# Optimization experiments

Measured on AMD Instinct MI355X. Metric: run time of the kernel, lower is better.

Reference implementation:

```python
import jax, jax.numpy as jnp
import numpy as np

HIDDEN = 1024
HEADS = 16
HEAD_DIM = HIDDEN // HEADS
LN_EPS = 1e-5


def setup_inputs() -> dict:
    key = jax.random.key(0)
    ks = jax.random.split(key, 8)
    B, S = 4, 2048
    s = 1.0 / np.sqrt(HIDDEN)
    return {
        "x": jax.random.normal(ks[0], (B, S, HIDDEN), dtype=jnp.float32),
        "Wq": jax.random.normal(ks[1], (HIDDEN, HIDDEN), dtype=jnp.float32) * s,
        "bq": jax.random.normal(ks[2], (HIDDEN,), dtype=jnp.float32) * 0.01,
        "Wk": jax.random.normal(ks[3], (HIDDEN, HIDDEN), dtype=jnp.float32) * s,
        "bk": jax.random.normal(ks[4], (HIDDEN,), dtype=jnp.float32) * 0.01,
        "Wv": jax.random.normal(ks[5], (HIDDEN, HIDDEN), dtype=jnp.float32) * s,
        "bv": jax.random.normal(ks[6], (HIDDEN,), dtype=jnp.float32) * 0.01,
        "gamma": jnp.ones((HIDDEN,), dtype=jnp.float32),
        "beta": jnp.zeros((HIDDEN,), dtype=jnp.float32),
    }


def reference(x, Wq, bq, Wk, bk, Wv, bv, gamma, beta):
    B, S, H = x.shape
    # LayerNorm
    mu = jnp.mean(x, axis=-1, keepdims=True)
    var = jnp.mean(jnp.square(x - mu), axis=-1, keepdims=True)
    xn = (x - mu) / jnp.sqrt(var + LN_EPS) * gamma + beta
    # QKV projections -> [B, heads, S, head_dim]
    def split_heads(t):
        return t.reshape(B, S, HEADS, HEAD_DIM).transpose(0, 2, 1, 3)
    q = split_heads(xn @ Wq + bq)
    k = split_heads(xn @ Wk + bk)
    v = split_heads(xn @ Wv + bv)
    scores = jnp.einsum("bhqd,bhkd->bhqk", q, k) / np.sqrt(HEAD_DIM)
    probs = jax.nn.softmax(scores, axis=-1)
    attended = jnp.einsum("bhqk,bhkd->bhqd", probs, v)
    attended = attended.transpose(0, 2, 1, 3).reshape(B, S, H)
    # residual (dropout = 0.0 / eval mode is identity)
    return xn + attended
```

## Files before the change

kernel.cpp:

```cpp
#include <hip/hip_runtime.h>
#include <hip/hip_bf16.h>

#define HIDDEN 1024
#define HEADS 16
#define HEAD_DIM 64
#define SEQ 2048
#define BATCH 4

typedef __attribute__((ext_vector_type(8))) short bf16x8;
typedef __attribute__((ext_vector_type(4))) float f32x4;
typedef __attribute__((ext_vector_type(16))) float f32x16;
typedef __attribute__((ext_vector_type(4))) short short4v;

static __device__ __forceinline__ unsigned short f2bf(float f) {
  union { float f; unsigned u; } u;
  u.f = f;
  unsigned r = u.u + 0x7fffu + ((u.u >> 16) & 1u);
  return (unsigned short)(r >> 16);
}

static __device__ __forceinline__ unsigned packtr(float lo, float hi) {
  union { float f; unsigned u; } a, b;
  a.f = lo; b.f = hi;
#if __has_builtin(__builtin_amdgcn_perm)
  return __builtin_amdgcn_perm(b.u, a.u, 0x07060302u);
#else
  return (b.u & 0xFFFF0000u) | (a.u >> 16);
#endif
}

static __device__ __forceinline__ bf16x8 frag4(unsigned u0, unsigned u1,
                                               unsigned u2, unsigned u3) {
  union { unsigned u[4]; bf16x8 v; } t;
  t.u[0] = u0; t.u[1] = u1; t.u[2] = u2; t.u[3] = u3;
  return t.v;
}

static __device__ __forceinline__ float fexp2(float x) {
#if __has_builtin(__builtin_amdgcn_exp2f)
  return __builtin_amdgcn_exp2f(x);
#else
  return exp2f(x);
#endif
}

typedef const __attribute__((address_space(1))) unsigned int* gp1_t;
typedef __attribute__((address_space(3))) unsigned int* lp3_t;
static __device__ __forceinline__ void gload_lds16(const void* g, void* l) {
  __builtin_amdgcn_global_load_lds((gp1_t)g, (lp3_t)l, 16, 0, 0);
}

__global__ __launch_bounds__(256) void wtrans_kernel(
    const float* __restrict__ Wq, const float* __restrict__ Wk,
    const float* __restrict__ Wv, unsigned short* __restrict__ Wt) {
  __shared__ float tile[64][65];
  int z = blockIdx.z;
  const float* W = (z == 0) ? Wq : (z == 1) ? Wk : Wv;
  int k0 = blockIdx.x * 64, n0 = blockIdx.y * 64;
  int tid = threadIdx.x;
  int tr = tid >> 4;
  int tc = tid & 15;
#pragma unroll
  for (int p = 0; p < 4; ++p) {
    int kk = p * 16 + tr;
    float4 v = *(const float4*)(W + (size_t)(k0 + kk) * HIDDEN + n0 + tc * 4);
    tile[kk][tc * 4 + 0] = v.x; tile[kk][tc * 4 + 1] = v.y;
    tile[kk][tc * 4 + 2] = v.z; tile[kk][tc * 4 + 3] = v.w;
  }
  __syncthreads();
  unsigned short* op = Wt + (size_t)z * HIDDEN * HIDDEN;
#pragma unroll
  for (int p = 0; p < 4; ++p) {
    int nn = p * 16 + tr;
    short4v o;
    o.x = (short)f2bf(tile[tc * 4 + 0][nn]);
    o.y = (short)f2bf(tile[tc * 4 + 1][nn]);
    o.z = (short)f2bf(tile[tc * 4 + 2][nn]);
    o.w = (short)f2bf(tile[tc * 4 + 3][nn]);
    *(short4v*)(op + (size_t)(n0 + nn) * HIDDEN + k0 + tc * 4) = o;
  }
}

__global__ __launch_bounds__(256) void ln_kernel(
    const float* __restrict__ x, const float* __restrict__ gamma,
    const float* __restrict__ beta, float* __restrict__ out,
    unsigned short* __restrict__ xnb) {
  int row = blockIdx.x;
  int tid = threadIdx.x;
  const float4* xr = (const float4*)(x + (size_t)row * HIDDEN);
  float4 v = xr[tid];
  float s = v.x + v.y + v.z + v.w;
  float sq = v.x * v.x + v.y * v.y + v.z * v.z + v.w * v.w;
#pragma unroll
  for (int off = 32; off >= 1; off >>= 1) {
    s += __shfl_xor(s, off);
    sq += __shfl_xor(sq, off);
  }
  __shared__ float red[8];
  int wave = tid >> 6, lane = tid & 63;
  if (lane == 0) { red[wave] = s; red[4 + wave] = sq; }
  __syncthreads();
  s = red[0] + red[1] + red[2] + red[3];
  sq = red[4] + red[5] + red[6] + red[7];
  float mu = s * (1.0f / HIDDEN);
  float var = sq * (1.0f / HIDDEN) - mu * mu;
  float rstd = rsqrtf(var + 1e-5f);
  float4 g = ((const float4*)gamma)[tid];
  float4 bt = ((const float4*)beta)[tid];
  float4 o;
  o.x = (v.x - mu) * rstd * g.x + bt.x;
  o.y = (v.y - mu) * rstd * g.y + bt.y;
  o.z = (v.z - mu) * rstd * g.z + bt.z;
  o.w = (v.w - mu) * rstd * g.w + bt.w;
  ((float4*)(out + (size_t)row * HIDDEN))[tid] = o;
  short4v p;
  p.x = (short)f2bf(o.x); p.y = (short)f2bf(o.y);
  p.z = (short)f2bf(o.z); p.w = (short)f2bf(o.w);
  *((short4v*)(xnb + (size_t)row * HIDDEN) + tid) = p;
}

__global__ __launch_bounds__(256) void qkv_gemm(
    const unsigned short* __restrict__ xnb, const unsigned short* __restrict__ Wt,
    const float* __restrict__ bq, const float* __restrict__ bk,
    const float* __restrict__ bv, unsigned short* __restrict__ qO,
    unsigned short* __restrict__ kO, unsigned short* __restrict__ vtO) {
  __shared__ unsigned short As[2][128 * 64];
  __shared__ unsigned short Bs[2][128 * 64];
  int z = blockIdx.z;
  int m0 = blockIdx.x * 128;
  int n0 = blockIdx.y * 128;
  int tid = threadIdx.x;
  int wave = tid >> 6, lane = tid & 63;
  int lr = lane & 15, g = lane >> 4;
  int wm = wave >> 1, wn = wave & 1;
  const unsigned short* Ab = xnb + (size_t)m0 * HIDDEN;
  const unsigned short* Bb = Wt + (size_t)z * HIDDEN * HIDDEN + (size_t)n0 * HIDDEN;
  int srow = wave * 8 + (lane >> 3);
  int scol = ((lane & 7) ^ (lane >> 3)) << 3;
  f32x4 acc[4][4];
#pragma unroll
  for (int i = 0; i < 4; ++i)
#pragma unroll
    for (int j = 0; j < 4; ++j) acc[i][j] = (f32x4){0.f, 0.f, 0.f, 0.f};

#pragma unroll
  for (int i = 0; i < 4; ++i) {
    int row = i * 32 + srow;
    gload_lds16(Ab + (size_t)row * HIDDEN + scol, &As[0][(i * 32 + wave * 8) * 64]);
    gload_lds16(Bb + (size_t)row * HIDDEN + scol, &Bs[0][(i * 32 + wave * 8) * 64]);
  }
  __syncthreads();

#pragma unroll 1
  for (int t = 0; t < 16; ++t) {
    int cur = t & 1;
    if (t < 15) {
      int k1 = (t + 1) * 64;
#pragma unroll
      for (int i = 0; i < 4; ++i) {
        int row = i * 32 + srow;
        gload_lds16(Ab + (size_t)row * HIDDEN + k1 + scol, &As[cur ^ 1][(i * 32 + wave * 8) * 64]);
        gload_lds16(Bb + (size_t)row * HIDDEN + k1 + scol, &Bs[cur ^ 1][(i * 32 + wave * 8) * 64]);
      }
    }
    bf16x8 aF[4][2], bF[4][2];
#pragma unroll
    for (int mb = 0; mb < 4; ++mb) {
      int row = wm * 64 + mb * 16 + lr;
#pragma unroll
      for (int ks = 0; ks < 2; ++ks)
        aF[mb][ks] = *(const bf16x8*)&As[cur][row * 64 + (((ks * 4 + g) ^ (row & 7)) << 3)];
    }
#pragma unroll
    for (int nb = 0; nb < 4; ++nb) {
      int row = wn * 64 + nb * 16 + lr;
#pragma unroll
      for (int ks = 0; ks < 2; ++ks)
        bF[nb][ks] = *(const bf16x8*)&Bs[cur][row * 64 + (((ks * 4 + g) ^ (row & 7)) << 3)];
    }
#pragma unroll
    for (int ks = 0; ks < 2; ++ks)
#pragma unroll
      for (int mb = 0; mb < 4; ++mb)
#pragma unroll
        for (int nb = 0; nb < 4; ++nb)
          acc[mb][nb] = __builtin_amdgcn_mfma_f32_16x16x32_bf16(aF[mb][ks], bF[nb][ks], acc[mb][nb], 0, 0, 0);
    __syncthreads();
  }
  const float* bias = (z == 0) ? bq : (z == 1) ? bk : bv;
  if (z == 2) {
#pragma unroll
    for (int nb = 0; nb < 4; ++nb) {
      int n = n0 + wn * 64 + nb * 16 + lr;
      float bsv = bias[n];
      int h = n >> 6, d = n & 63;
#pragma unroll
      for (int mb = 0; mb < 4; ++mb) {
        int m = m0 + wm * 64 + mb * 16 + g * 4;
        int bb = m >> 11, sIdx = m & 2047;
        short4v pk;
        pk.x = (short)f2bf(acc[mb][nb][0] + bsv);
        pk.y = (short)f2bf(acc[mb][nb][1] + bsv);
        pk.z = (short)f2bf(acc[mb][nb][2] + bsv);
        pk.w = (short)f2bf(acc[mb][nb][3] + bsv);
        *(short4v*)(vtO + (size_t)((bb * HEADS + h) * HEAD_DIM + d) * SEQ + sIdx) = pk;
      }
    }
  } else {
    unsigned short* outp = (z == 0) ? qO : kO;
    float scale = (z == 0) ? 0.18033688011112042f : 1.0f;
#pragma unroll
    for (int nb = 0; nb < 4; ++nb) {
      int n = n0 + wn * 64 + nb * 16 + lr;
      float bsv = bias[n];
      int h = n >> 6, d = n & 63;
#pragma unroll
      for (int mb = 0; mb < 4; ++mb) {
#pragma unroll
        for (int r = 0; r < 4; ++r) {
          int m = m0 + wm * 64 + mb * 16 + g * 4 + r;
          int bb = m >> 11, sIdx = m & 2047;
          unsigned short bits = f2bf((acc[mb][nb][r] + bsv) * scale);
          outp[(size_t)((bb * HEADS + h) * SEQ + sIdx) * HEAD_DIM + d] = bits;
        }
      }
    }
  }
}

static __device__ __forceinline__ void attn_subtile(
    const unsigned short* __restrict__ Kb, const unsigned short* __restrict__ Vb,
    const int (&koff)[4], const bf16x8 (&qF)[4],
    const f32x16& ZERO, f32x16& o0, f32x16& o1, float& lsum) {
  f32x16 sc0, sc1;
  __builtin_amdgcn_s_setprio(1);
  {
    bf16x8 k0 = *(const bf16x8*)&Kb[koff[0]];
    bf16x8 k1 = *(const bf16x8*)&Kb[koff[0] + 256];
    sc0 = __builtin_amdgcn_mfma_f32_32x32x16_bf16(k0, qF[0], ZERO, 0, 0, 0);
    sc1 = __builtin_amdgcn_mfma_f32_32x32x16_bf16(k1, qF[0], ZERO, 0, 0, 0);
  }
#pragma unroll
  for (int s = 1; s < 4; ++s) {
    bf16x8 k0 = *(const bf16x8*)&Kb[koff[s]];
    bf16x8 k1 = *(const bf16x8*)&Kb[koff[s] + 256];
    sc0 = __builtin_amdgcn_mfma_f32_32x32x16_bf16(k0, qF[s], sc0, 0, 0, 0);
    sc1 = __builtin_amdgcn_mfma_f32_32x32x16_bf16(k1, qF[s], sc1, 0, 0, 0);
  }
  __builtin_amdgcn_s_setprio(0);
#pragma unroll
  for (int s = 0; s < 4; ++s) {
    float e[8];
#pragma unroll
    for (int j = 0; j < 8; ++j) {
      float scv = (s < 2) ? sc0[8 * s + j] : sc1[8 * (s - 2) + j];
      e[j] = fexp2(scv);
    }
    lsum += ((e[0] + e[1]) + (e[2] + e[3])) + ((e[4] + e[5]) + (e[6] + e[7]));
    unsigned pa0 = packtr(e[0], e[1]);
    unsigned pb0 = packtr(e[2], e[3]);
    unsigned pa1 = packtr(e[4], e[5]);
    unsigned pb1 = packtr(e[6], e[7]);
#if __has_builtin(__builtin_amdgcn_permlane32_swap)
    auto ra = __builtin_amdgcn_permlane32_swap(pa0, pa1, false, false);
    auto rb = __builtin_amdgcn_permlane32_swap(pb0, pb1, false, false);
    bf16x8 pF = frag4(ra[0], rb[0], ra[1], rb[1]);
#else
    int hf = (threadIdx.x & 63) >> 5;
    unsigned t0 = __shfl_xor(hf ? pa0 : pa1, 32);
    unsigned t1 = __shfl_xor(hf ? pb0 : pb1, 32);
    bf16x8 pF = frag4(hf ? t0 : pa0, hf ? t1 : pb0,
                      hf ? pa1 : t0, hf ? pb1 : t1);
#endif
    bf16x8 v0 = *(const bf16x8*)&Vb[koff[s]];
    bf16x8 v1 = *(const bf16x8*)&Vb[koff[s] + 256];
    __builtin_amdgcn_s_setprio(1);
    o0 = __builtin_amdgcn_mfma_f32_32x32x16_bf16(v0, pF, o0, 0, 0, 0);
    o1 = __builtin_amdgcn_mfma_f32_32x32x16_bf16(v1, pF, o1, 0, 0, 0);
    __builtin_amdgcn_s_setprio(0);
  }
}

__global__ __launch_bounds__(512, 4) void attn_kernel(
    const unsigned short* __restrict__ qB, const unsigned short* __restrict__ kB,
    const unsigned short* __restrict__ vtB, float* __restrict__ out) {
  __shared__ unsigned short Kt[2][2][64 * 64];
  __shared__ unsigned short Vt[2][2][64 * 64];
  int orig = blockIdx.y * gridDim.x + blockIdx.x;
  int swz = (orig & 7) * 64 + (orig >> 3);
  int bx = swz & 7;
  int by = swz >> 3;
  int b = by >> 4, hh = by & 15;
  int tid = threadIdx.x, wave = tid >> 6, lane = tid & 63;
  int lq = lane & 31;
  int hf = lane >> 5;
  int q0 = bx * 256 + wave * 32;
  const unsigned short* qh = qB + (size_t)by * SEQ * HEAD_DIM;
  const unsigned short* kh = kB + (size_t)by * SEQ * HEAD_DIM;
  const unsigned short* vh = vtB + (size_t)by * HEAD_DIM * SEQ;

  bf16x8 qF[4];
#pragma unroll
  for (int s = 0; s < 4; ++s)
    qF[s] = *(const bf16x8*)(qh + (size_t)(q0 + lq) * HEAD_DIM + s * 16 + hf * 8);

  int koff[4];
#pragma unroll
  for (int s = 0; s < 4; ++s)
    koff[s] = (2 * s + hf) * 512 + lq * 8;

  f32x16 o0, o1, ZERO;
#pragma unroll
  for (int r = 0; r < 16; ++r) { o0[r] = 0.f; o1[r] = 0.f; ZERO[r] = 0.f; }
  float lsum = 0.f;

#pragma unroll
  for (int sub = 0; sub < 2; ++sub) {
    gload_lds16(kh + (size_t)(sub * 64 + lane) * HEAD_DIM + wave * 8, &Kt[0][sub][wave * 512]);
    gload_lds16(vh + (size_t)lane * SEQ + sub * 64 + wave * 8, &Vt[0][sub][wave * 512]);
  }
  __syncthreads();

#pragma unroll 1
  for (int t = 0; t < 16; ++t) {
    int cur = t & 1;
    if (t < 15) {
      int kv1 = (t + 1) * 128;
#pragma unroll
      for (int sub = 0; sub < 2; ++sub) {
        gload_lds16(kh + (size_t)(kv1 + sub * 64 + lane) * HEAD_DIM + wave * 8,
                    &Kt[cur ^ 1][sub][wave * 512]);
        gload_lds16(vh + (size_t)lane * SEQ + kv1 + sub * 64 + wave * 8,
                    &Vt[cur ^ 1][sub][wave * 512]);
      }
    }
    attn_subtile(Kt[cur][0], Vt[cur][0], koff, qF, ZERO, o0, o1, lsum);
    attn_subtile(Kt[cur][1], Vt[cur][1], koff, qF, ZERO, o0, o1, lsum);
    __syncthreads();
  }
  lsum += __shfl_xor(lsum, 32);
  float inv = 1.0f / lsum;
  float* orow = out + ((size_t)b * SEQ + q0 + lq) * HIDDEN + hh * HEAD_DIM;
#pragma unroll
  for (int r = 0; r < 16; ++r) {
    int d0 = (r & 3) + 8 * (r >> 2) + 4 * hf;
    orow[d0] += o0[r] * inv;
    orow[32 + d0] += o1[r] * inv;
  }
}

extern "C" void kernel_launch(void* const* d_in, const int* in_sizes, int n_in,
                              void* d_out, int out_size, void* d_ws, size_t ws_size,
                              hipStream_t stream) {
  const float* x     = (const float*)d_in[0];
  const float* Wq    = (const float*)d_in[1];
  const float* bq    = (const float*)d_in[2];
  const float* Wk    = (const float*)d_in[3];
  const float* bk    = (const float*)d_in[4];
  const float* Wv    = (const float*)d_in[5];
  const float* bv    = (const float*)d_in[6];
  const float* gamma = (const float*)d_in[7];
  const float* beta  = (const float*)d_in[8];
  float* out = (float*)d_out;
  char* ws = (char*)d_ws;
  const size_t MB = 1024 * 1024;
  unsigned short* xnb = (unsigned short*)(ws);
  unsigned short* Wt  = (unsigned short*)(ws + 16 * MB);
  unsigned short* qb  = (unsigned short*)(ws + 22 * MB);
  unsigned short* kb  = (unsigned short*)(ws + 38 * MB);
  unsigned short* vtb = (unsigned short*)(ws + 54 * MB);

  hipLaunchKernelGGL(wtrans_kernel, dim3(16, 16, 3), dim3(256), 0, stream, Wq, Wk, Wv, Wt);
  hipLaunchKernelGGL(ln_kernel, dim3(BATCH * SEQ), dim3(256), 0, stream, x, gamma, beta, out, xnb);
  hipLaunchKernelGGL(qkv_gemm, dim3(64, 8, 3), dim3(256), 0, stream, xnb, Wt, bq, bk, bv, qb, kb, vtb);
  hipLaunchKernelGGL(attn_kernel, dim3(8, 64), dim3(512), 0, stream, qb, kb, vtb, out);
}
```

Before: 167.5 us.

## Triple-buffer K/V tiles with swizzled LDS layout and partial vmcnt waits

```diff
diff --git a/kernel.cpp b/kernel.cpp
--- a/kernel.cpp
+++ b/kernel.cpp
@@ -228,64 +228,11 @@
   }
 }
 
-static __device__ __forceinline__ void attn_subtile(
-    const unsigned short* __restrict__ Kb, const unsigned short* __restrict__ Vb,
-    const int (&koff)[4], const bf16x8 (&qF)[4],
-    const f32x16& ZERO, f32x16& o0, f32x16& o1, float& lsum) {
-  f32x16 sc0, sc1;
-  __builtin_amdgcn_s_setprio(1);
-  {
-    bf16x8 k0 = *(const bf16x8*)&Kb[koff[0]];
-    bf16x8 k1 = *(const bf16x8*)&Kb[koff[0] + 256];
-    sc0 = __builtin_amdgcn_mfma_f32_32x32x16_bf16(k0, qF[0], ZERO, 0, 0, 0);
-    sc1 = __builtin_amdgcn_mfma_f32_32x32x16_bf16(k1, qF[0], ZERO, 0, 0, 0);
-  }
-#pragma unroll
-  for (int s = 1; s < 4; ++s) {
-    bf16x8 k0 = *(const bf16x8*)&Kb[koff[s]];
-    bf16x8 k1 = *(const bf16x8*)&Kb[koff[s] + 256];
-    sc0 = __builtin_amdgcn_mfma_f32_32x32x16_bf16(k0, qF[s], sc0, 0, 0, 0);
-    sc1 = __builtin_amdgcn_mfma_f32_32x32x16_bf16(k1, qF[s], sc1, 0, 0, 0);
-  }
-  __builtin_amdgcn_s_setprio(0);
-#pragma unroll
-  for (int s = 0; s < 4; ++s) {
-    float e[8];
-#pragma unroll
-    for (int j = 0; j < 8; ++j) {
-      float scv = (s < 2) ? sc0[8 * s + j] : sc1[8 * (s - 2) + j];
-      e[j] = fexp2(scv);
-    }
-    lsum += ((e[0] + e[1]) + (e[2] + e[3])) + ((e[4] + e[5]) + (e[6] + e[7]));
-    unsigned pa0 = packtr(e[0], e[1]);
-    unsigned pb0 = packtr(e[2], e[3]);
-    unsigned pa1 = packtr(e[4], e[5]);
-    unsigned pb1 = packtr(e[6], e[7]);
-#if __has_builtin(__builtin_amdgcn_permlane32_swap)
-    auto ra = __builtin_amdgcn_permlane32_swap(pa0, pa1, false, false);
-    auto rb = __builtin_amdgcn_permlane32_swap(pb0, pb1, false, false);
-    bf16x8 pF = frag4(ra[0], rb[0], ra[1], rb[1]);
-#else
-    int hf = (threadIdx.x & 63) >> 5;
-    unsigned t0 = __shfl_xor(hf ? pa0 : pa1, 32);
-    unsigned t1 = __shfl_xor(hf ? pb0 : pb1, 32);
-    bf16x8 pF = frag4(hf ? t0 : pa0, hf ? t1 : pb0,
-                      hf ? pa1 : t0, hf ? pb1 : t1);
-#endif
-    bf16x8 v0 = *(const bf16x8*)&Vb[koff[s]];
-    bf16x8 v1 = *(const bf16x8*)&Vb[koff[s] + 256];
-    __builtin_amdgcn_s_setprio(1);
-    o0 = __builtin_amdgcn_mfma_f32_32x32x16_bf16(v0, pF, o0, 0, 0, 0);
-    o1 = __builtin_amdgcn_mfma_f32_32x32x16_bf16(v1, pF, o1, 0, 0, 0);
-    __builtin_amdgcn_s_setprio(0);
-  }
-}
-
 __global__ __launch_bounds__(512, 4) void attn_kernel(
     const unsigned short* __restrict__ qB, const unsigned short* __restrict__ kB,
     const unsigned short* __restrict__ vtB, float* __restrict__ out) {
-  __shared__ unsigned short Kt[2][2][64 * 64];
-  __shared__ unsigned short Vt[2][2][64 * 64];
+  __shared__ unsigned short Kt[3][64 * 64];
+  __shared__ unsigned short Vt[3][64 * 64];
   int orig = blockIdx.y * gridDim.x + blockIdx.x;
   int swz = (orig & 7) * 64 + (orig >> 3);
   int bx = swz & 7;
@@ -304,10 +251,13 @@
   for (int s = 0; s < 4; ++s)
     qF[s] = *(const bf16x8*)(qh + (size_t)(q0 + lq) * HEAD_DIM + s * 16 + hf * 8);
 
+  int srow = wave * 8 + (lane >> 3);
+  int scoff = ((lane & 7) ^ (lane >> 3)) << 3;
+  int xorb = (lq & 7) << 4;
   int koff[4];
 #pragma unroll
   for (int s = 0; s < 4; ++s)
-    koff[s] = (2 * s + hf) * 512 + lq * 8;
+    koff[s] = (lq * 128 + ((s * 32 + hf * 16) ^ xorb)) >> 1;
 
   f32x16 o0, o1, ZERO;
 #pragma unroll
@@ -315,28 +265,78 @@
   float lsum = 0.f;
 
 #pragma unroll
-  for (int sub = 0; sub < 2; ++sub) {
-    gload_lds16(kh + (size_t)(sub * 64 + lane) * HEAD_DIM + wave * 8, &Kt[0][sub][wave * 512]);
-    gload_lds16(vh + (size_t)lane * SEQ + sub * 64 + wave * 8, &Vt[0][sub][wave * 512]);
-  }
-  __syncthreads();
+  for (int tt = 0; tt < 2; ++tt) {
+    gload_lds16(kh + (size_t)(tt * 64 + srow) * HEAD_DIM + scoff, &Kt[tt][wave * 512]);
+    gload_lds16(vh + (size_t)srow * SEQ + tt * 64 + scoff, &Vt[tt][wave * 512]);
+  }
+  asm volatile("s_waitcnt vmcnt(2)" ::: "memory");
+  __builtin_amdgcn_s_barrier();
+  asm volatile("" ::: "memory");
 
 #pragma unroll 1
-  for (int t = 0; t < 16; ++t) {
-    int cur = t & 1;
-    if (t < 15) {
-      int kv1 = (t + 1) * 128;
-#pragma unroll
-      for (int sub = 0; sub < 2; ++sub) {
-        gload_lds16(kh + (size_t)(kv1 + sub * 64 + lane) * HEAD_DIM + wave * 8,
-                    &Kt[cur ^ 1][sub][wave * 512]);
-        gload_lds16(vh + (size_t)lane * SEQ + kv1 + sub * 64 + wave * 8,
-                    &Vt[cur ^ 1][sub][wave * 512]);
+  for (int t = 0; t < 32; ++t) {
+    int cur = t % 3;
+    if (t < 30) {
+      int nb = cur + 2; if (nb >= 3) nb -= 3;
+      int kv = (t + 2) * 64;
+      gload_lds16(kh + (size_t)(kv + srow) * HEAD_DIM + scoff, &Kt[nb][wave * 512]);
+      gload_lds16(vh + (size_t)srow * SEQ + kv + scoff, &Vt[nb][wave * 512]);
+    }
+    const unsigned short* Kb = Kt[cur];
+    const unsigned short* Vb = Vt[cur];
+    f32x16 sc0, sc1;
+    __builtin_amdgcn_s_setprio(1);
+    {
+      bf16x8 k0 = *(const bf16x8*)&Kb[koff[0]];
+      bf16x8 k1 = *(const bf16x8*)&Kb[koff[0] + 2048];
+      sc0 = __builtin_amdgcn_mfma_f32_32x32x16_bf16(k0, qF[0], ZERO, 0, 0, 0);
+      sc1 = __builtin_amdgcn_mfma_f32_32x32x16_bf16(k1, qF[0], ZERO, 0, 0, 0);
+    }
+#pragma unroll
+    for (int s = 1; s < 4; ++s) {
+      bf16x8 k0 = *(const bf16x8*)&Kb[koff[s]];
+      bf16x8 k1 = *(const bf16x8*)&Kb[koff[s] + 2048];
+      sc0 = __builtin_amdgcn_mfma_f32_32x32x16_bf16(k0, qF[s], sc0, 0, 0, 0);
+      sc1 = __builtin_amdgcn_mfma_f32_32x32x16_bf16(k1, qF[s], sc1, 0, 0, 0);
+    }
+    __builtin_amdgcn_s_setprio(0);
+#pragma unroll
+    for (int s = 0; s < 4; ++s) {
+      float e[8];
+#pragma unroll
+      for (int j = 0; j < 8; ++j) {
+        float scv = (s < 2) ? sc0[8 * s + j] : sc1[8 * (s - 2) + j];
+        e[j] = fexp2(scv);
       }
-    }
-    attn_subtile(Kt[cur][0], Vt[cur][0], koff, qF, ZERO, o0, o1, lsum);
-    attn_subtile(Kt[cur][1], Vt[cur][1], koff, qF, ZERO, o0, o1, lsum);
-    __syncthreads();
+      lsum += ((e[0] + e[1]) + (e[2] + e[3])) + ((e[4] + e[5]) + (e[6] + e[7]));
+      unsigned pa0 = packtr(e[0], e[1]);
+      unsigned pb0 = packtr(e[2], e[3]);
+      unsigned pa1 = packtr(e[4], e[5]);
+      unsigned pb1 = packtr(e[6], e[7]);
+#if __has_builtin(__builtin_amdgcn_permlane32_swap)
+      auto ra = __builtin_amdgcn_permlane32_swap(pa0, pa1, false, false);
+      auto rb = __builtin_amdgcn_permlane32_swap(pb0, pb1, false, false);
+      bf16x8 pF = frag4(ra[0], rb[0], ra[1], rb[1]);
+#else
+      unsigned t0 = __shfl_xor(hf ? pa0 : pa1, 32);
+      unsigned t1 = __shfl_xor(hf ? pb0 : pb1, 32);
+      bf16x8 pF = frag4(hf ? t0 : pa0, hf ? t1 : pb0,
+                        hf ? pa1 : t0, hf ? pb1 : t1);
+#endif
+      bf16x8 v0 = *(const bf16x8*)&Vb[koff[s]];
+      bf16x8 v1 = *(const bf16x8*)&Vb[koff[s] + 2048];
+      __builtin_amdgcn_s_setprio(1);
+      o0 = __builtin_amdgcn_mfma_f32_32x32x16_bf16(v0, pF, o0, 0, 0, 0);
+      o1 = __builtin_amdgcn_mfma_f32_32x32x16_bf16(v1, pF, o1, 0, 0, 0);
+      __builtin_amdgcn_s_setprio(0);
+    }
+    if (t < 30) {
+      asm volatile("s_waitcnt vmcnt(2)" ::: "memory");
+    } else {
+      asm volatile("s_waitcnt vmcnt(0)" ::: "memory");
+    }
+    __builtin_amdgcn_s_barrier();
+    asm volatile("" ::: "memory");
   }
   lsum += __shfl_xor(lsum, 32);
   float inv = 1.0f / lsum;
```

New measurement: 165.9 us. Within noise of the previous version (-0.9%).

## Merge LN and weight transpose kernels, swizzle K/V LDS, fuse residual store

Applied to the files above, without the earlier changes.

```diff
diff --git a/kernel.cpp b/kernel.cpp
--- a/kernel.cpp
+++ b/kernel.cpp
@@ -17,6 +17,12 @@
   u.f = f;
   unsigned r = u.u + 0x7fffu + ((u.u >> 16) & 1u);
   return (unsigned short)(r >> 16);
+}
+
+static __device__ __forceinline__ float bf2f(short s) {
+  union { unsigned u; float f; } t;
+  t.u = ((unsigned)(unsigned short)s) << 16;
+  return t.f;
 }
 
 static __device__ __forceinline__ unsigned packtr(float lo, float hi) {
@@ -50,73 +56,68 @@
   __builtin_amdgcn_global_load_lds((gp1_t)g, (lp3_t)l, 16, 0, 0);
 }
 
-__global__ __launch_bounds__(256) void wtrans_kernel(
+__global__ __launch_bounds__(256) void prep_kernel(
+    const float* __restrict__ x, const float* __restrict__ gamma,
+    const float* __restrict__ beta, unsigned short* __restrict__ xnb,
     const float* __restrict__ Wq, const float* __restrict__ Wk,
     const float* __restrict__ Wv, unsigned short* __restrict__ Wt) {
   __shared__ float tile[64][65];
-  int z = blockIdx.z;
-  const float* W = (z == 0) ? Wq : (z == 1) ? Wk : Wv;
-  int k0 = blockIdx.x * 64, n0 = blockIdx.y * 64;
+  int bid = blockIdx.x;
   int tid = threadIdx.x;
-  int tr = tid >> 4;
-  int tc = tid & 15;
-#pragma unroll
-  for (int p = 0; p < 4; ++p) {
-    int kk = p * 16 + tr;
-    float4 v = *(const float4*)(W + (size_t)(k0 + kk) * HIDDEN + n0 + tc * 4);
-    tile[kk][tc * 4 + 0] = v.x; tile[kk][tc * 4 + 1] = v.y;
-    tile[kk][tc * 4 + 2] = v.z; tile[kk][tc * 4 + 3] = v.w;
-  }
-  __syncthreads();
-  unsigned short* op = Wt + (size_t)z * HIDDEN * HIDDEN;
-#pragma unroll
-  for (int p = 0; p < 4; ++p) {
-    int nn = p * 16 + tr;
-    short4v o;
-    o.x = (short)f2bf(tile[tc * 4 + 0][nn]);
-    o.y = (short)f2bf(tile[tc * 4 + 1][nn]);
-    o.z = (short)f2bf(tile[tc * 4 + 2][nn]);
-    o.w = (short)f2bf(tile[tc * 4 + 3][nn]);
-    *(short4v*)(op + (size_t)(n0 + nn) * HIDDEN + k0 + tc * 4) = o;
-  }
-}
-
-__global__ __launch_bounds__(256) void ln_kernel(
-    const float* __restrict__ x, const float* __restrict__ gamma,
-    const float* __restrict__ beta, float* __restrict__ out,
-    unsigned short* __restrict__ xnb) {
-  int row = blockIdx.x;
-  int tid = threadIdx.x;
-  const float4* xr = (const float4*)(x + (size_t)row * HIDDEN);
-  float4 v = xr[tid];
-  float s = v.x + v.y + v.z + v.w;
-  float sq = v.x * v.x + v.y * v.y + v.z * v.z + v.w * v.w;
-#pragma unroll
-  for (int off = 32; off >= 1; off >>= 1) {
-    s += __shfl_xor(s, off);
-    sq += __shfl_xor(sq, off);
-  }
-  __shared__ float red[8];
-  int wave = tid >> 6, lane = tid & 63;
-  if (lane == 0) { red[wave] = s; red[4 + wave] = sq; }
-  __syncthreads();
-  s = red[0] + red[1] + red[2] + red[3];
-  sq = red[4] + red[5] + red[6] + red[7];
-  float mu = s * (1.0f / HIDDEN);
-  float var = sq * (1.0f / HIDDEN) - mu * mu;
-  float rstd = rsqrtf(var + 1e-5f);
-  float4 g = ((const float4*)gamma)[tid];
-  float4 bt = ((const float4*)beta)[tid];
-  float4 o;
-  o.x = (v.x - mu) * rstd * g.x + bt.x;
-  o.y = (v.y - mu) * rstd * g.y + bt.y;
-  o.z = (v.z - mu) * rstd * g.z + bt.z;
-  o.w = (v.w - mu) * rstd * g.w + bt.w;
-  ((float4*)(out + (size_t)row * HIDDEN))[tid] = o;
-  short4v p;
-  p.x = (short)f2bf(o.x); p.y = (short)f2bf(o.y);
-  p.z = (short)f2bf(o.z); p.w = (short)f2bf(o.w);
-  *((short4v*)(xnb + (size_t)row * HIDDEN) + tid) = p;
+  if (bid < BATCH * SEQ) {
+    int row = bid;
+    const float4* xr = (const float4*)(x + (size_t)row * HIDDEN);
+    float4 v = xr[tid];
+    float s = v.x + v.y + v.z + v.w;
+    float sq = v.x * v.x + v.y * v.y + v.z * v.z + v.w * v.w;
+#pragma unroll
+    for (int off = 32; off >= 1; off >>= 1) {
+      s += __shfl_xor(s, off);
+      sq += __shfl_xor(sq, off);
+    }
+    int wave = tid >> 6, lane = tid & 63;
+    if (lane == 0) { tile[0][wave] = s; tile[0][4 + wave] = sq; }
+    __syncthreads();
+    s = tile[0][0] + tile[0][1] + tile[0][2] + tile[0][3];
+    sq = tile[0][4] + tile[0][5] + tile[0][6] + tile[0][7];
+    float mu = s * (1.0f / HIDDEN);
+    float var = sq * (1.0f / HIDDEN) - mu * mu;
+    float rstd = rsqrtf(var + 1e-5f);
+    float4 g = ((const float4*)gamma)[tid];
+    float4 bt = ((const float4*)beta)[tid];
+    short4v p;
+    p.x = (short)f2bf((v.x - mu) * rstd * g.x + bt.x);
+    p.y = (short)f2bf((v.y - mu) * rstd * g.y + bt.y);
+    p.z = (short)f2bf((v.z - mu) * rstd * g.z + bt.z);
+    p.w = (short)f2bf((v.w - mu) * rstd * g.w + bt.w);
+    *((short4v*)(xnb + (size_t)row * HIDDEN) + tid) = p;
+  } else {
+    int w = bid - BATCH * SEQ;
+    int z = w >> 8, rem = w & 255;
+    int k0 = (rem & 15) * 64, n0 = (rem >> 4) * 64;
+    const float* W = (z == 0) ? Wq : (z == 1) ? Wk : Wv;
+    int tr = tid >> 4;
+    int tc = tid & 15;
+#pragma unroll
+    for (int p = 0; p < 4; ++p) {
+      int kk = p * 16 + tr;
+      float4 v = *(const float4*)(W + (size_t)(k0 + kk) * HIDDEN + n0 + tc * 4);
+      tile[kk][tc * 4 + 0] = v.x; tile[kk][tc * 4 + 1] = v.y;
+      tile[kk][tc * 4 + 2] = v.z; tile[kk][tc * 4 + 3] = v.w;
+    }
+    __syncthreads();
+    unsigned short* op = Wt + (size_t)z * HIDDEN * HIDDEN;
+#pragma unroll
+    for (int p = 0; p < 4; ++p) {
+      int nn = p * 16 + tr;
+      short4v o;
+      o.x = (short)f2bf(tile[tc * 4 + 0][nn]);
+      o.y = (short)f2bf(tile[tc * 4 + 1][nn]);
+      o.z = (short)f2bf(tile[tc * 4 + 2][nn]);
+      o.w = (short)f2bf(tile[tc * 4 + 3][nn]);
+      *(short4v*)(op + (size_t)(n0 + nn) * HIDDEN + k0 + tc * 4) = o;
+    }
+  }
 }
 
 __global__ __launch_bounds__(256) void qkv_gemm(
@@ -236,14 +237,14 @@
   __builtin_amdgcn_s_setprio(1);
   {
     bf16x8 k0 = *(const bf16x8*)&Kb[koff[0]];
-    bf16x8 k1 = *(const bf16x8*)&Kb[koff[0] + 256];
+    bf16x8 k1 = *(const bf16x8*)&Kb[koff[0] + 2048];
     sc0 = __builtin_amdgcn_mfma_f32_32x32x16_bf16(k0, qF[0], ZERO, 0, 0, 0);
     sc1 = __builtin_amdgcn_mfma_f32_32x32x16_bf16(k1, qF[0], ZERO, 0, 0, 0);
   }
 #pragma unroll
   for (int s = 1; s < 4; ++s) {
     bf16x8 k0 = *(const bf16x8*)&Kb[koff[s]];
-    bf16x8 k1 = *(const bf16x8*)&Kb[koff[s] + 256];
+    bf16x8 k1 = *(const bf16x8*)&Kb[koff[s] + 2048];
     sc0 = __builtin_amdgcn_mfma_f32_32x32x16_bf16(k0, qF[s], sc0, 0, 0, 0);
     sc1 = __builtin_amdgcn_mfma_f32_32x32x16_bf16(k1, qF[s], sc1, 0, 0, 0);
   }
@@ -273,7 +274,7 @@
                       hf ? pa1 : t0, hf ? pb1 : t1);
 #endif
     bf16x8 v0 = *(const bf16x8*)&Vb[koff[s]];
-    bf16x8 v1 = *(const bf16x8*)&Vb[koff[s] + 256];
+    bf16x8 v1 = *(const bf16x8*)&Vb[koff[s] + 2048];
     __builtin_amdgcn_s_setprio(1);
     o0 = __builtin_amdgcn_mfma_f32_32x32x16_bf16(v0, pF, o0, 0, 0, 0);
     o1 = __builtin_amdgcn_mfma_f32_32x32x16_bf16(v1, pF, o1, 0, 0, 0);
@@ -283,7 +284,8 @@
 
 __global__ __launch_bounds__(512, 4) void attn_kernel(
     const unsigned short* __restrict__ qB, const unsigned short* __restrict__ kB,
-    const unsigned short* __restrict__ vtB, float* __restrict__ out) {
+    const unsigned short* __restrict__ vtB, const unsigned short* __restrict__ xnb,
+    float* __restrict__ out) {
   __shared__ unsigned short Kt[2][2][64 * 64];
   __shared__ unsigned short Vt[2][2][64 * 64];
   int orig = blockIdx.y * gridDim.x + blockIdx.x;
@@ -304,10 +306,13 @@
   for (int s = 0; s < 4; ++s)
     qF[s] = *(const bf16x8*)(qh + (size_t)(q0 + lq) * HEAD_DIM + s * 16 + hf * 8);
 
+  int srow = wave * 8 + (lane >> 3);
+  int scoff = ((lane & 7) ^ (lane >> 3)) << 3;
+  int xorb = (lq & 7) << 4;
   int koff[4];
 #pragma unroll
   for (int s = 0; s < 4; ++s)
-    koff[s] = (2 * s + hf) * 512 + lq * 8;
+    koff[s] = (lq * 128 + ((s * 32 + hf * 16) ^ xorb)) >> 1;
 
   f32x16 o0, o1, ZERO;
 #pragma unroll
@@ -316,8 +321,8 @@
 
 #pragma unroll
   for (int sub = 0; sub < 2; ++sub) {
-    gload_lds16(kh + (size_t)(sub * 64 + lane) * HEAD_DIM + wave * 8, &Kt[0][sub][wave * 512]);
-    gload_lds16(vh + (size_t)lane * SEQ + sub * 64 + wave * 8, &Vt[0][sub][wave * 512]);
+    gload_lds16(kh + (size_t)(sub * 64 + srow) * HEAD_DIM + scoff, &Kt[0][sub][wave * 512]);
+    gload_lds16(vh + (size_t)srow * SEQ + sub * 64 + scoff, &Vt[0][sub][wave * 512]);
   }
   __syncthreads();
 
@@ -328,9 +333,9 @@
       int kv1 = (t + 1) * 128;
 #pragma unroll
       for (int sub = 0; sub < 2; ++sub) {
-        gload_lds16(kh + (size_t)(kv1 + sub * 64 + lane) * HEAD_DIM + wave * 8,
+        gload_lds16(kh + (size_t)(kv1 + sub * 64 + srow) * HEAD_DIM + scoff,
                     &Kt[cur ^ 1][sub][wave * 512]);
-        gload_lds16(vh + (size_t)lane * SEQ + kv1 + sub * 64 + wave * 8,
+        gload_lds16(vh + (size_t)srow * SEQ + kv1 + sub * 64 + scoff,
                     &Vt[cur ^ 1][sub][wave * 512]);
       }
     }
@@ -340,12 +345,25 @@
   }
   lsum += __shfl_xor(lsum, 32);
   float inv = 1.0f / lsum;
-  float* orow = out + ((size_t)b * SEQ + q0 + lq) * HIDDEN + hh * HEAD_DIM;
-#pragma unroll
-  for (int r = 0; r < 16; ++r) {
-    int d0 = (r & 3) + 8 * (r >> 2) + 4 * hf;
-    orow[d0] += o0[r] * inv;
-    orow[32 + d0] += o1[r] * inv;
+  size_t rowbase = ((size_t)b * SEQ + q0 + lq) * HIDDEN + hh * HEAD_DIM;
+  const unsigned short* xrow = xnb + rowbase;
+  float* orow = out + rowbase;
+#pragma unroll
+  for (int qd = 0; qd < 4; ++qd) {
+    int d0 = qd * 8 + 4 * hf;
+    short4v xa = *(const short4v*)(xrow + d0);
+    short4v xb = *(const short4v*)(xrow + 32 + d0);
+    float4 oa, ob;
+    oa.x = bf2f(xa.x) + o0[qd * 4 + 0] * inv;
+    oa.y = bf2f(xa.y) + o0[qd * 4 + 1] * inv;
+    oa.z = bf2f(xa.z) + o0[qd * 4 + 2] * inv;
+    oa.w = bf2f(xa.w) + o0[qd * 4 + 3] * inv;
+    ob.x = bf2f(xb.x) + o1[qd * 4 + 0] * inv;
+    ob.y = bf2f(xb.y) + o1[qd * 4 + 1] * inv;
+    ob.z = bf2f(xb.z) + o1[qd * 4 + 2] * inv;
+    ob.w = bf2f(xb.w) + o1[qd * 4 + 3] * inv;
+    *(float4*)(orow + d0) = oa;
+    *(float4*)(orow + 32 + d0) = ob;
   }
 }
 
@@ -370,8 +388,8 @@
   unsigned short* kb  = (unsigned short*)(ws + 38 * MB);
   unsigned short* vtb = (unsigned short*)(ws + 54 * MB);
 
-  hipLaunchKernelGGL(wtrans_kernel, dim3(16, 16, 3), dim3(256), 0, stream, Wq, Wk, Wv, Wt);
-  hipLaunchKernelGGL(ln_kernel, dim3(BATCH * SEQ), dim3(256), 0, stream, x, gamma, beta, out, xnb);
+  hipLaunchKernelGGL(prep_kernel, dim3(BATCH * SEQ + 768), dim3(256), 0, stream,
+                     x, gamma, beta, xnb, Wq, Wk, Wv, Wt);
   hipLaunchKernelGGL(qkv_gemm, dim3(64, 8, 3), dim3(256), 0, stream, xnb, Wt, bq, bk, bv, qb, kb, vtb);
-  hipLaunchKernelGGL(attn_kernel, dim3(8, 64), dim3(512), 0, stream, qb, kb, vtb, out);
-}
+  hipLaunchKernelGGL(attn_kernel, dim3(8, 64), dim3(512), 0, stream, qb, kb, vtb, xnb, out);
+}
```

Result: faster. 158.1 us (-5.6%).
